# Performance work log

Hardware: AMD Instinct MI355X
Metric: run time of the kernel (lower is better)

## Reference

```python
import jax, jax.numpy as jnp
import numpy as np
from jax import lax


def setup_inputs() -> dict:
    key = jax.random.key(0)
    k1, k2, k3, k4, k5 = jax.random.split(key, 5)
    B, C_in, H, W = 32768, 3, 14, 14
    C_out, kh, kw = 16, 5, 5
    num_outputs = 1000
    return {
        "feature_map": jax.random.normal(k1, (B, C_in, H, W), dtype=jnp.float32),
        "conv_w": jax.random.normal(k2, (C_out, C_in, kh, kw), dtype=jnp.float32),
        "conv_b": jax.random.normal(k3, (C_out,), dtype=jnp.float32),
        "lin_w": jax.random.normal(k4, (num_outputs, C_out * 5 * 5), dtype=jnp.float32),
        "lin_b": jax.random.normal(k5, (num_outputs,), dtype=jnp.float32),
    }


def reference(feature_map, conv_w, conv_b, lin_w, lin_b):
    # Conv2D: valid cross-correlation, stride 1, no padding (B,Ci,H,W)x(Co,Ci,h,w)->(B,Co,H-h+1,W-w+1)
    y = lax.conv_general_dilated(
        feature_map, conv_w, window_strides=(1, 1), padding="VALID",
        dimension_numbers=("NCHW", "OIHW", "NCHW"))
    y = jax.nn.relu(y + conv_b[None, :, None, None])
    # Non-overlapping 2x2 max pool: (B,C,10,10) -> (B,C,5,5)
    B, C, H, W = y.shape
    y = y.reshape(B, C, H // 2, 2, W // 2, 2).max(axis=(3, 5))
    # Linear head on flattened features (B, C*5*5) -> (B, num_outputs)
    out = y.reshape(B, -1) @ lin_w.T + lin_b
    return out
```

## Files before the change

### kernel.cpp

```cpp
#include <hip/hip_runtime.h>
#include <stdint.h>

#define BTOT 32768
#define NIMG 16
#define KF   416

typedef __attribute__((ext_vector_type(2))) _Float16 half2r;
typedef __attribute__((ext_vector_type(8))) short short8;
typedef __attribute__((ext_vector_type(4))) float floatx4;

static __device__ __forceinline__ half2r u2h(unsigned int u) {
    return __builtin_bit_cast(half2r, u);
}
static __device__ __forceinline__ unsigned int h2u(half2r h) {
    return __builtin_bit_cast(unsigned int, h);
}
static __device__ __forceinline__ half2r cvt2h(float a, float b) {
    return __builtin_bit_cast(half2r, __builtin_amdgcn_cvt_pkrtz(a, b));
}
__device__ __forceinline__ unsigned short f2bf(float x) {
    union { float f; unsigned int u; } v; v.f = x;
    unsigned int r = v.u + 0x7fffu + ((v.u >> 16) & 1u);
    return (unsigned short)(r >> 16);
}

__global__ __launch_bounds__(256) void conv_pool_kernel(
    const float* __restrict__ fm, const float* __restrict__ cw,
    const float* __restrict__ cb, unsigned short* __restrict__ feat)
{
    __shared__ __align__(16) unsigned int s_img[NIMG * 294];
    __shared__ unsigned int s_w2[16 * 76];

    const int tid = threadIdx.x;
    const int b0 = blockIdx.x * NIMG;

    const float4* in4 = (const float4*)fm;
    for (int idx = tid; idx < NIMG * 147; idx += 256) {
        float4 v = in4[(size_t)b0 * 147 + idx];
        half2r lo = cvt2h(v.x, v.y);
        half2r hi = cvt2h(v.z, v.w);
        *(uint2*)&s_img[idx * 2] = make_uint2(h2u(lo), h2u(hi));
    }
    for (int idx = tid; idx < 1200; idx += 256) {
        int co = idx / 75;
        int r = idx - co * 75;
        float w = cw[idx];
        s_w2[co * 76 + r] = h2u(cvt2h(w, w));
    }
    __syncthreads();

    const int b_local = tid & 15;
    const int co = tid >> 4;
    const float bias = cb[co];
    const unsigned int* ibase = s_img + b_local * 294;
    const unsigned int* wbase = s_w2 + co * 76;
    unsigned short* fout = feat + (size_t)(b0 + b_local) * KF + co * 25;

    for (int r = 0; r < 5; ++r) {
        half2r acc0[5], acc1[5];
        #pragma unroll
        for (int p = 0; p < 5; ++p) { acc0[p] = u2h(0u); acc1[p] = u2h(0u); }

        #pragma unroll
        for (int ci = 0; ci < 3; ++ci) {
            const unsigned int* ip = ibase + ci * 98 + r * 14;
            unsigned int wr[25];
            #pragma unroll
            for (int k = 0; k < 25; ++k) wr[k] = wbase[ci * 25 + k];

            #pragma unroll
            for (int ir = 0; ir < 6; ++ir) {
                unsigned int v[7];
                #pragma unroll
                for (int q = 0; q < 7; ++q) v[q] = ip[ir * 7 + q];
                unsigned int s[6];
                #pragma unroll
                for (int q = 0; q < 6; ++q) s[q] = (v[q] >> 16) | (v[q + 1] << 16);

                if (ir < 5) {
                    #pragma unroll
                    for (int p = 0; p < 5; ++p) {
                        acc0[p] += u2h(v[p])     * u2h(wr[ir * 5 + 0]);
                        acc0[p] += u2h(s[p])     * u2h(wr[ir * 5 + 1]);
                        acc0[p] += u2h(v[p + 1]) * u2h(wr[ir * 5 + 2]);
                        acc0[p] += u2h(s[p + 1]) * u2h(wr[ir * 5 + 3]);
                        acc0[p] += u2h(v[p + 2]) * u2h(wr[ir * 5 + 4]);
                    }
                }
                if (ir >= 1) {
                    const int kh = ir - 1;
                    #pragma unroll
                    for (int p = 0; p < 5; ++p) {
                        acc1[p] += u2h(v[p])     * u2h(wr[kh * 5 + 0]);
                        acc1[p] += u2h(s[p])     * u2h(wr[kh * 5 + 1]);
                        acc1[p] += u2h(v[p + 1]) * u2h(wr[kh * 5 + 2]);
                        acc1[p] += u2h(s[p + 1]) * u2h(wr[kh * 5 + 3]);
                        acc1[p] += u2h(v[p + 2]) * u2h(wr[kh * 5 + 4]);
                    }
                }
            }
        }
        #pragma unroll
        for (int p = 0; p < 5; ++p) {
            float a = (float)acc0[p].x, b = (float)acc0[p].y;
            float c = (float)acc1[p].x, d = (float)acc1[p].y;
            float m = fmaxf(fmaxf(a, b), fmaxf(c, d)) + bias;
            m = fmaxf(m, 0.f);
            fout[r * 5 + p] = f2bf(m);
        }
    }
    if (co == 0) {
        uint4 z = make_uint4(0u, 0u, 0u, 0u);
        *(uint4*)(feat + (size_t)(b0 + b_local) * KF + 400) = z;
        *(uint4*)(feat + (size_t)(b0 + b_local) * KF + 408) = z;
    }
}

__global__ __launch_bounds__(256) void prep_w_kernel(const float* __restrict__ lw,
                                                     unsigned short* __restrict__ Wb)
{
    int c = blockIdx.x * 256 + threadIdx.x;
    if (c >= 1024 * 52) return;
    int n = c / 52;
    int kc = (c - n * 52) * 8;
    unsigned short v[8];
    #pragma unroll
    for (int j = 0; j < 8; ++j) {
        int k = kc + j;
        float x = (n < 1000 && k < 400) ? lw[n * 400 + k] : 0.f;
        v[j] = f2bf(x);
    }
    *(uint4*)(Wb + (size_t)n * KF + kc) = *(uint4*)v;
}

__global__ __launch_bounds__(256) void gemm_kernel(
    const unsigned short* __restrict__ F, const unsigned short* __restrict__ Wb,
    const float* __restrict__ lb, float* __restrict__ out)
{
    __shared__ __align__(16) unsigned short At[128 * 32];
    __shared__ __align__(16) unsigned short Bt[128 * 32];

    const int tid = threadIdx.x;
    const int bm = blockIdx.x >> 3;
    const int bn = blockIdx.x & 7;
    const int m0 = bm * 128;
    const int n0 = bn * 128;

    const int w = tid >> 6;
    const int lane = tid & 63;
    const int wm = w & 1, wn = w >> 1;
    const int lq = lane >> 4, ln = lane & 15;

    floatx4 zero = {0.f, 0.f, 0.f, 0.f};
    floatx4 acc[4][4];
    #pragma unroll
    for (int i = 0; i < 4; ++i)
        #pragma unroll
        for (int j = 0; j < 4; ++j) acc[i][j] = zero;

    const int srow = w * 16 + (lane >> 2);
    const int skc = (lane & 3) * 8;
    const unsigned short* gA = F + (size_t)(m0 + srow) * KF + skc;
    const unsigned short* gB = Wb + (size_t)(n0 + srow) * KF + skc;

    for (int kb = 0; kb < KF; kb += 32) {
        #pragma unroll
        for (int t = 0; t < 2; ++t) {
            __builtin_amdgcn_global_load_lds(
                (const __attribute__((address_space(1))) void*)(gA + (size_t)(t * 64) * KF + kb),
                (__attribute__((address_space(3))) void*)&At[(w * 16 + t * 64) * 32],
                16, 0, 0);
            __builtin_amdgcn_global_load_lds(
                (const __attribute__((address_space(1))) void*)(gB + (size_t)(t * 64) * KF + kb),
                (__attribute__((address_space(3))) void*)&Bt[(w * 16 + t * 64) * 32],
                16, 0, 0);
        }
        __syncthreads();
        short8 af[4], bf[4];
        #pragma unroll
        for (int i = 0; i < 4; ++i)
            af[i] = *(const short8*)&At[(wm * 64 + i * 16 + ln) * 32 + lq * 8];
        #pragma unroll
        for (int j = 0; j < 4; ++j)
            bf[j] = *(const short8*)&Bt[(wn * 64 + j * 16 + ln) * 32 + lq * 8];
        #pragma unroll
        for (int i = 0; i < 4; ++i)
            #pragma unroll
            for (int j = 0; j < 4; ++j)
                acc[i][j] = __builtin_amdgcn_mfma_f32_16x16x32_bf16(af[i], bf[j], acc[i][j], 0, 0, 0);
        __syncthreads();
    }

    #pragma unroll
    for (int j = 0; j < 4; ++j) {
        int n = n0 + wn * 64 + j * 16 + ln;
        if (n >= 1000) continue;
        float bias = lb[n];
        #pragma unroll
        for (int i = 0; i < 4; ++i) {
            int mb = m0 + wm * 64 + i * 16 + lq * 4;
            #pragma unroll
            for (int rr = 0; rr < 4; ++rr)
                out[(size_t)(mb + rr) * 1000 + n] = acc[i][j][rr] + bias;
        }
    }
}

extern "C" void kernel_launch(void* const* d_in, const int* in_sizes, int n_in,
                              void* d_out, int out_size, void* d_ws, size_t ws_size,
                              hipStream_t stream)
{
    const float* fm = (const float*)d_in[0];
    const float* cw = (const float*)d_in[1];
    const float* cb = (const float*)d_in[2];
    const float* lw = (const float*)d_in[3];
    const float* lb = (const float*)d_in[4];
    float* out = (float*)d_out;

    unsigned short* feat = (unsigned short*)d_ws;
    unsigned short* Wb   = (unsigned short*)d_ws + (size_t)BTOT * KF;

    prep_w_kernel<<<208, 256, 0, stream>>>(lw, Wb);
    conv_pool_kernel<<<BTOT / NIMG, 256, 0, stream>>>(fm, cw, cb, feat);
    gemm_kernel<<<2048, 256, 0, stream>>>(feat, Wb, lb, out);
}
```

Before: 334.5 us.

## Compute conv via bf16 MFMA im2col and stage pooled features in LDS

The conv+pool kernel drops packed-fp16 FMA arithmetic and computes the convolution with 16x16x32 bf16 MFMA instructions, using an im2col gather from LDS. The four pool positions of a 2x2 window map to the four accumulator rows, so max-pooling happens within each lane. Outputs are staged in shared memory and written to global memory with coalesced 16-byte stores, with the K padding zeroed in LDS. This cuts VALU work and scattered 2-byte global stores, at the cost of many scalar LDS gathers per MFMA and lower input precision (bf16 instead of fp16).

```diff
diff --git a/kernel.cpp b/kernel.cpp
--- a/kernel.cpp
+++ b/kernel.cpp
@@ -5,19 +5,9 @@
 #define NIMG 16
 #define KF   416
 
-typedef __attribute__((ext_vector_type(2))) _Float16 half2r;
 typedef __attribute__((ext_vector_type(8))) short short8;
 typedef __attribute__((ext_vector_type(4))) float floatx4;
 
-static __device__ __forceinline__ half2r u2h(unsigned int u) {
-    return __builtin_bit_cast(half2r, u);
-}
-static __device__ __forceinline__ unsigned int h2u(half2r h) {
-    return __builtin_bit_cast(unsigned int, h);
-}
-static __device__ __forceinline__ half2r cvt2h(float a, float b) {
-    return __builtin_bit_cast(half2r, __builtin_amdgcn_cvt_pkrtz(a, b));
-}
 __device__ __forceinline__ unsigned short f2bf(float x) {
     union { float f; unsigned int u; } v; v.f = x;
     unsigned int r = v.u + 0x7fffu + ((v.u >> 16) & 1u);
@@ -28,92 +18,92 @@
     const float* __restrict__ fm, const float* __restrict__ cw,
     const float* __restrict__ cb, unsigned short* __restrict__ feat)
 {
-    __shared__ __align__(16) unsigned int s_img[NIMG * 294];
-    __shared__ unsigned int s_w2[16 * 76];
-
-    const int tid = threadIdx.x;
-    const int b0 = blockIdx.x * NIMG;
-
-    const float4* in4 = (const float4*)fm;
+    __shared__ __align__(16) unsigned short s_img[NIMG * 588];
+    __shared__ __align__(16) unsigned short s_out[NIMG * 416];
+
+    const int tid  = threadIdx.x;
+    const int b0   = blockIdx.x * NIMG;
+    const int lane = tid & 63;
+    const int wave = tid >> 6;
+
+    const float4* in4 = (const float4*)(fm + (size_t)b0 * 588);
     for (int idx = tid; idx < NIMG * 147; idx += 256) {
-        float4 v = in4[(size_t)b0 * 147 + idx];
-        half2r lo = cvt2h(v.x, v.y);
-        half2r hi = cvt2h(v.z, v.w);
-        *(uint2*)&s_img[idx * 2] = make_uint2(h2u(lo), h2u(hi));
-    }
-    for (int idx = tid; idx < 1200; idx += 256) {
-        int co = idx / 75;
-        int r = idx - co * 75;
-        float w = cw[idx];
-        s_w2[co * 76 + r] = h2u(cvt2h(w, w));
-    }
+        float4 v = in4[idx];
+        unsigned int u0 = (unsigned int)f2bf(v.x) | ((unsigned int)f2bf(v.y) << 16);
+        unsigned int u1 = (unsigned int)f2bf(v.z) | ((unsigned int)f2bf(v.w) << 16);
+        *(uint2*)&s_img[idx * 4] = make_uint2(u0, u1);
+    }
+    {
+        int img = tid >> 4, k = tid & 15;
+        s_out[img * 416 + 400 + k] = 0;
+    }
+
+    const int co = lane & 15;
+    const int q  = lane >> 4;
+
+    union U8 { unsigned short h[8]; short8 v; };
+    U8 bw[3];
+    #pragma unroll
+    for (int ci = 0; ci < 3; ++ci) {
+        #pragma unroll
+        for (int j = 0; j < 8; ++j) {
+            int t = q * 8 + j;
+            bw[ci].h[j] = (t < 25) ? f2bf(cw[co * 75 + ci * 25 + t]) : (unsigned short)0;
+        }
+    }
+    const float bias = cb[co];
+
+    int hoff[8];
+    #pragma unroll
+    for (int j = 0; j < 8; ++j) {
+        int t = q * 8 + j;
+        int kh = t / 5;
+        hoff[j] = (t < 25) ? (kh * 14 + (t - kh * 5)) : 0;
+    }
+
+    const int r  = lane & 15;
+    const int qd = r >> 2;
+    const int cy = (r >> 1) & 1;
+    const int cx = r & 1;
+
     __syncthreads();
 
-    const int b_local = tid & 15;
-    const int co = tid >> 4;
-    const float bias = cb[co];
-    const unsigned int* ibase = s_img + b_local * 294;
-    const unsigned int* wbase = s_w2 + co * 76;
-    unsigned short* fout = feat + (size_t)(b0 + b_local) * KF + co * 25;
-
-    for (int r = 0; r < 5; ++r) {
-        half2r acc0[5], acc1[5];
-        #pragma unroll
-        for (int p = 0; p < 5; ++p) { acc0[p] = u2h(0u); acc1[p] = u2h(0u); }
-
+    const unsigned short* sw = s_img + wave * 4 * 588;
+    unsigned short* ow = s_out + wave * 4 * 416;
+
+    for (int t = 0; t < 25; ++t) {
+        int g   = t * 4 + qd;
+        int img = (g * 41) >> 10;
+        int q25 = g - img * 25;
+        int qy  = (q25 * 13) >> 6;
+        int qx  = q25 - qy * 5;
+        const unsigned short* p = sw + img * 588 + (qy * 2 + cy) * 14 + (qx * 2 + cx);
+
+        floatx4 acc = {0.f, 0.f, 0.f, 0.f};
         #pragma unroll
         for (int ci = 0; ci < 3; ++ci) {
-            const unsigned int* ip = ibase + ci * 98 + r * 14;
-            unsigned int wr[25];
+            union { unsigned int u[4]; short8 v; } a;
             #pragma unroll
-            for (int k = 0; k < 25; ++k) wr[k] = wbase[ci * 25 + k];
-
-            #pragma unroll
-            for (int ir = 0; ir < 6; ++ir) {
-                unsigned int v[7];
-                #pragma unroll
-                for (int q = 0; q < 7; ++q) v[q] = ip[ir * 7 + q];
-                unsigned int s[6];
-                #pragma unroll
-                for (int q = 0; q < 6; ++q) s[q] = (v[q] >> 16) | (v[q + 1] << 16);
-
-                if (ir < 5) {
-                    #pragma unroll
-                    for (int p = 0; p < 5; ++p) {
-                        acc0[p] += u2h(v[p])     * u2h(wr[ir * 5 + 0]);
-                        acc0[p] += u2h(s[p])     * u2h(wr[ir * 5 + 1]);
-                        acc0[p] += u2h(v[p + 1]) * u2h(wr[ir * 5 + 2]);
-                        acc0[p] += u2h(s[p + 1]) * u2h(wr[ir * 5 + 3]);
-                        acc0[p] += u2h(v[p + 2]) * u2h(wr[ir * 5 + 4]);
-                    }
-                }
-                if (ir >= 1) {
-                    const int kh = ir - 1;
-                    #pragma unroll
-                    for (int p = 0; p < 5; ++p) {
-                        acc1[p] += u2h(v[p])     * u2h(wr[kh * 5 + 0]);
-                        acc1[p] += u2h(s[p])     * u2h(wr[kh * 5 + 1]);
-                        acc1[p] += u2h(v[p + 1]) * u2h(wr[kh * 5 + 2]);
-                        acc1[p] += u2h(s[p + 1]) * u2h(wr[kh * 5 + 3]);
-                        acc1[p] += u2h(v[p + 2]) * u2h(wr[kh * 5 + 4]);
-                    }
-                }
+            for (int pp = 0; pp < 4; ++pp) {
+                unsigned int lo = p[ci * 196 + hoff[2 * pp]];
+                unsigned int hi = p[ci * 196 + hoff[2 * pp + 1]];
+                a.u[pp] = lo | (hi << 16);
             }
-        }
-        #pragma unroll
-        for (int p = 0; p < 5; ++p) {
-            float a = (float)acc0[p].x, b = (float)acc0[p].y;
-            float c = (float)acc1[p].x, d = (float)acc1[p].y;
-            float m = fmaxf(fmaxf(a, b), fmaxf(c, d)) + bias;
-            m = fmaxf(m, 0.f);
-            fout[r * 5 + p] = f2bf(m);
-        }
-    }
-    if (co == 0) {
-        uint4 z = make_uint4(0u, 0u, 0u, 0u);
-        *(uint4*)(feat + (size_t)(b0 + b_local) * KF + 400) = z;
-        *(uint4*)(feat + (size_t)(b0 + b_local) * KF + 408) = z;
-    }
+            acc = __builtin_amdgcn_mfma_f32_16x16x32_bf16(a.v, bw[ci].v, acc, 0, 0, 0);
+        }
+
+        int gd   = t * 4 + q;
+        int imgd = (gd * 41) >> 10;
+        int q25d = gd - imgd * 25;
+        float m = fmaxf(fmaxf(acc[0], acc[1]), fmaxf(acc[2], acc[3])) + bias;
+        ow[imgd * 416 + co * 25 + q25d] = f2bf(fmaxf(m, 0.f));
+    }
+
+    __syncthreads();
+    const uint4* so4 = (const uint4*)s_out;
+    uint4* fo4 = (uint4*)(feat + (size_t)b0 * KF);
+    for (int idx = tid; idx < NIMG * 52; idx += 256)
+        fo4[idx] = so4[idx];
 }
 
 __global__ __launch_bounds__(256) void prep_w_kernel(const float* __restrict__ lw,
```

Result: faster. 319.4 us (-4.5%).
